# Kernel tuning notes

Hardware: AMD Instinct MI355X
Metric: run time of the kernel (lower is better)

Reference implementation:

```python
import jax, jax.numpy as jnp
import numpy as np

TAU = 2.0        # leak time constant
CLAMP = 1000.0   # state clamp in LeakyRNN.recurrence
EPS = 1e-4       # eps in PolicyRNN.evaluate

B, T, H, NI, NA = 64, 2048, 256, 4, 2


def setup_inputs() -> dict:
    key = jax.random.key(0)
    ks = jax.random.split(key, 10)
    state = jax.random.normal(ks[0], (B, T, NI), jnp.float32)
    last_action = jax.random.normal(ks[1], (B, T, NA), jnp.float32)
    reward = jax.random.randint(ks[2], (B, T, NA), 0, 2).astype(jnp.float32)
    hidden_in = jnp.zeros((B, H), jnp.float32)
    W1 = jax.random.normal(ks[3], (H, NI + 2 * NA), jnp.float32) * np.float32(np.sqrt(2.0 / (NI + 2 * NA)))
    b1 = jnp.zeros((H,), jnp.float32)
    Wih = jax.random.normal(ks[4], (H, H), jnp.float32) * np.float32(np.sqrt(2.0 / H))
    Whh_raw = jax.random.normal(ks[5], (H, H), jnp.float32) * np.float32(0.5 / np.sqrt(H))
    W2 = jax.random.normal(ks[6], (H, H), jnp.float32) * np.float32(np.sqrt(2.0 / H))
    b2 = jnp.zeros((H,), jnp.float32)
    W3 = jax.random.normal(ks[7], (NA, H), jnp.float32) * np.float32(np.sqrt(2.0 / H))
    b3 = jnp.zeros((NA,), jnp.float32)
    Qs = jax.random.normal(ks[8], (B, T, NA), jnp.float32)
    # MultLayerAdaptiveSimple with alphas=[1,0]: weight1=[1,0], weight2=[0,1]
    mix_w = jnp.array([[1.0, 0.0], [0.0, 1.0]], jnp.float32)
    return dict(state=state, last_action=last_action, reward=reward,
                hidden_in=hidden_in, W1=W1, b1=b1, Wih=Wih, Whh_raw=Whh_raw,
                W2=W2, b2=b2, W3=W3, b3=b3, Qs=Qs, mix_w=mix_w)


def reference(state, last_action, reward, hidden_in, W1, b1, Wih, Whh_raw,
              W2, b2, W3, b3, Qs, mix_w):
    # (B,T,.) -> (T,B,.) time-major, matching permute(1,0,2)
    x = jnp.concatenate([reward, state, last_action], -1).transpose(1, 0, 2)
    x = jax.nn.relu(x @ W1.T + b1)                     # linear1 + relu

    # IdentityDiagonal parametrization: zero diagonal, subtract I/tau
    Whh = Whh_raw - jnp.diag(jnp.diag(Whh_raw)) - jnp.eye(H, dtype=Whh_raw.dtype) / TAU
    u = x @ Wih.T                                      # precompute input drive (T,B,H)
    leak = 1.0 - 1.0 / TAU

    def step(h, ut):
        h_new = jnp.clip(leak * h + ut + jax.nn.relu(h) @ Whh.T, -CLAMP, CLAMP)
        return h_new, h_new

    hidden_out, ys = jax.lax.scan(step, hidden_in, u)  # ys: (T,B,H)

    y = jax.nn.relu(ys @ W2.T + b2) @ W3.T + b3        # linear2+relu, linear3
    probs = y.transpose(1, 0, 2)                       # (B,T,NA)

    # evaluate() deterministic path with reward-indexed adaptive mixing
    z = (probs == 0.0).astype(probs.dtype) * EPS
    logp = jnp.log(jax.nn.softmax(probs, -1) + z)
    logq = jnp.log(jax.nn.softmax(Qs, -1) + z)
    # SumOne parametrization (p=1) on each MultLayer 2-vector
    w = jnp.clip(mix_w, -1.0, 1.0)
    table = w / jnp.sum(jnp.abs(w), axis=1, keepdims=True)   # (2,2)
    sel = table[reward[:, :, 0].astype(jnp.int32)]           # (B,T,2)
    mixed = logp * sel[..., :1] + logq * sel[..., 1:2]
    return jnp.exp(mixed), hidden_out
```

## Files before the change

kernel.cpp:

```cpp
#include <hip/hip_runtime.h>
#include <hip/hip_bf16.h>
#include <math.h>

#define Bn 64
#define Tn 2048
#define Hn 256

constexpr float LEAK    = 0.5f;
constexpr float NEGDIAG = -0.5f;
constexpr float CLAMP_V = 1000.0f;
constexpr float EPS_V   = 1e-4f;

typedef __attribute__((ext_vector_type(8))) short  short8;
typedef __attribute__((ext_vector_type(4))) float  f32x4;
typedef __attribute__((ext_vector_type(2))) float  f32x2;

#define FAST_BARRIER() do {                                   \
    asm volatile("s_waitcnt lgkmcnt(0)" ::: "memory");        \
    __builtin_amdgcn_s_barrier();                             \
    asm volatile("" ::: "memory");                            \
  } while (0)

__device__ inline short bf16_rne(float x) {
  __hip_bfloat16 h = __float2bfloat16(x);
  return *reinterpret_cast<short*>(&h);
}
__device__ inline float bf16_to_f(short s) {
  union { unsigned u; float f; } c; c.u = ((unsigned)(unsigned short)s) << 16;
  return c.f;
}
__device__ inline unsigned pack2(short a, short b) {
  return (unsigned)(unsigned short)a | ((unsigned)(unsigned short)b << 16);
}
__device__ inline void pkfma(f32x2& a, f32x2 x, f32x2 y) {
  asm("v_pk_fma_f32 %0, %1, %2, %0" : "+v"(a) : "v"(x), "v"(y));
}
#define SWZ(x, imm) __int_as_float(__builtin_amdgcn_ds_swizzle(__float_as_int(x), (imm)))

#define SA 40

__global__ __launch_bounds__(512) void g_u(
    const float* __restrict__ reward, const float* __restrict__ state,
    const float* __restrict__ last_action, const float* __restrict__ W1,
    const float* __restrict__ b1, const float* __restrict__ Wih,
    float* __restrict__ u)
{
  __shared__ short Ah[128*SA], Al[128*SA], Bh[256*SA], Bl[256*SA];
  __shared__ __align__(16) float inp_s[128][8];
  __shared__ __align__(16) float w1_s[256][8];
  __shared__ float b1_s[256];
  const int tid = threadIdx.x;
  const int r0  = blockIdx.x * 128;

  for (int idx = tid; idx < 2048; idx += 512) ((float*)w1_s)[idx] = W1[idx];
  if (tid < 256) b1_s[tid] = b1[tid];
  for (int idx = tid; idx < 1024; idx += 512) {
    int rr = idx >> 3, i = idx & 7;
    int r = r0 + rr, b = r & 63, t = r >> 6;
    long base = (long)b * Tn + t;
    float v;
    if (i < 2)      v = reward[base * 2 + i];
    else if (i < 6) v = state[base * 4 + (i - 2)];
    else            v = last_action[base * 2 + (i - 6)];
    inp_s[rr][i] = v;
  }

  const int w    = tid >> 6, lane = tid & 63;
  const int wm   = w >> 2, wn = w & 3;
  const int fr   = lane & 15, fk = lane >> 4;
  f32x4 acc[4][4];
  #pragma unroll
  for (int a = 0; a < 4; ++a)
    #pragma unroll
    for (int c = 0; c < 4; ++c) acc[a][c] = (f32x4){0.f, 0.f, 0.f, 0.f};

  __syncthreads();

  for (int ks = 0; ks < 8; ++ks) {
    const int k0 = ks * 32;
    if (ks) __syncthreads();
    for (int p = tid; p < 2048; p += 512) {
      int rr = p >> 4, kp = (p & 15) * 2;
      int k = k0 + kp;
      float4 iv0 = *reinterpret_cast<const float4*>(&inp_s[rr][0]);
      float4 iv1 = *reinterpret_cast<const float4*>(&inp_s[rr][4]);
      float4 wa0 = *reinterpret_cast<const float4*>(&w1_s[k][0]);
      float4 wa1 = *reinterpret_cast<const float4*>(&w1_s[k][4]);
      float4 wb0 = *reinterpret_cast<const float4*>(&w1_s[k+1][0]);
      float4 wb1 = *reinterpret_cast<const float4*>(&w1_s[k+1][4]);
      float s0 = b1_s[k], s1 = b1_s[k+1];
      s0 = fmaf(iv0.x, wa0.x, s0); s0 = fmaf(iv0.y, wa0.y, s0);
      s0 = fmaf(iv0.z, wa0.z, s0); s0 = fmaf(iv0.w, wa0.w, s0);
      s0 = fmaf(iv1.x, wa1.x, s0); s0 = fmaf(iv1.y, wa1.y, s0);
      s0 = fmaf(iv1.z, wa1.z, s0); s0 = fmaf(iv1.w, wa1.w, s0);
      s1 = fmaf(iv0.x, wb0.x, s1); s1 = fmaf(iv0.y, wb0.y, s1);
      s1 = fmaf(iv0.z, wb0.z, s1); s1 = fmaf(iv0.w, wb0.w, s1);
      s1 = fmaf(iv1.x, wb1.x, s1); s1 = fmaf(iv1.y, wb1.y, s1);
      s1 = fmaf(iv1.z, wb1.z, s1); s1 = fmaf(iv1.w, wb1.w, s1);
      float v0 = fmaxf(s0, 0.f), v1 = fmaxf(s1, 0.f);
      short h0 = bf16_rne(v0), h1 = bf16_rne(v1);
      short l0 = bf16_rne(v0 - bf16_to_f(h0)), l1 = bf16_rne(v1 - bf16_to_f(h1));
      int off = rr * SA + kp;
      *reinterpret_cast<unsigned*>(&Ah[off]) = pack2(h0, h1);
      *reinterpret_cast<unsigned*>(&Al[off]) = pack2(l0, l1);
    }
    for (int c = tid; c < 2048; c += 512) {
      int n = c >> 3, kc = (c & 7) * 4;
      float4 f = *reinterpret_cast<const float4*>(&Wih[n * 256 + k0 + kc]);
      short h0 = bf16_rne(f.x), h1 = bf16_rne(f.y), h2 = bf16_rne(f.z), h3 = bf16_rne(f.w);
      short l0 = bf16_rne(f.x - bf16_to_f(h0)), l1 = bf16_rne(f.y - bf16_to_f(h1));
      short l2 = bf16_rne(f.z - bf16_to_f(h2)), l3 = bf16_rne(f.w - bf16_to_f(h3));
      int off = n * SA + kc;
      *reinterpret_cast<uint2*>(&Bh[off]) = make_uint2(pack2(h0, h1), pack2(h2, h3));
      *reinterpret_cast<uint2*>(&Bl[off]) = make_uint2(pack2(l0, l1), pack2(l2, l3));
    }
    __syncthreads();
    short8 bhf[4], blf[4];
    #pragma unroll
    for (int nf = 0; nf < 4; ++nf) {
      const int brow = wn * 64 + nf * 16 + fr;
      bhf[nf] = *reinterpret_cast<const short8*>(&Bh[brow * SA + fk * 8]);
      blf[nf] = *reinterpret_cast<const short8*>(&Bl[brow * SA + fk * 8]);
    }
    #pragma unroll
    for (int mf = 0; mf < 4; ++mf) {
      const int arow = wm * 64 + mf * 16 + fr;
      short8 ah = *reinterpret_cast<const short8*>(&Ah[arow * SA + fk * 8]);
      short8 al = *reinterpret_cast<const short8*>(&Al[arow * SA + fk * 8]);
      #pragma unroll
      for (int nf = 0; nf < 4; ++nf) {
        acc[mf][nf] = __builtin_amdgcn_mfma_f32_16x16x32_bf16(ah, bhf[nf], acc[mf][nf], 0, 0, 0);
        acc[mf][nf] = __builtin_amdgcn_mfma_f32_16x16x32_bf16(ah, blf[nf], acc[mf][nf], 0, 0, 0);
        acc[mf][nf] = __builtin_amdgcn_mfma_f32_16x16x32_bf16(al, bhf[nf], acc[mf][nf], 0, 0, 0);
      }
    }
  }
  #pragma unroll
  for (int mf = 0; mf < 4; ++mf) {
    const int rbase = r0 + wm * 64 + mf * 16 + (lane >> 4) * 4;
    #pragma unroll
    for (int nf = 0; nf < 4; ++nf) {
      const int n = wn * 64 + nf * 16 + fr;
      #pragma unroll
      for (int j = 0; j < 4; ++j)
        u[(long)(rbase + j) * Hn + n] = acc[mf][nf][j];
    }
  }
}

__global__ __launch_bounds__(1024, 4) void k_scan(
    const float* __restrict__ Whh_raw, const float* __restrict__ hidden_in,
    float* __restrict__ ubuf, float* __restrict__ out)
{
  __shared__ __align__(16) float rh[2][256];
  const int tid = threadIdx.x;
  const int w = tid >> 6;
  const int l = tid & 63;
  const int g = l & 15;
  const int o = l >> 4;
  const int b = blockIdx.x;
  const int kbase = g << 4;

  f32x2 w2[4][8];
  #pragma unroll
  for (int m = 0; m < 4; ++m) {
    const int j = (w << 4) + (o << 2) + m;
    #pragma unroll
    for (int i = 0; i < 8; ++i) {
      const int k = kbase + i * 2;
      float a = Whh_raw[j * 256 + k];
      float c = Whh_raw[j * 256 + k + 1];
      if (k == j)     a = NEGDIAG;
      if (k + 1 == j) c = NEGDIAG;
      w2[m][i] = (f32x2){a, c};
    }
  }

  const int b0 = g & 1, b1 = (g >> 1) & 1;
  const bool owner = (g < 4);
  const int m_own = (b0 << 1) | b1;
  const int j_own = (w << 4) + (o << 2) + m_own;

  const int wr_off = (j_own & ~15) | ((((j_own >> 2) + (j_own >> 5)) & 3) << 2)
                   | (j_own & 3);
  int a_q[4];
  #pragma unroll
  for (int q = 0; q < 4; ++q) a_q[q] = kbase + (((((g >> 1) + q) & 3)) << 2);

  float h = 0.f, u_c = 0.f, u_n = 0.f;
  if (owner) {
    h   = hidden_in[b * Hn + j_own];
    u_c = ubuf[b * Hn + j_own];
    u_n = ubuf[((long)Bn + b) * Hn + j_own];
  }
  const float* u_ptr  = ubuf + ((long)2 * Bn + b) * Hn + j_own;
  float*       ys_ptr = ubuf + (long)b * Hn + j_own;

#define SCAN_STEP(P)                                                         \
  {                                                                          \
    if (owner) rh[P][wr_off] = fmaxf(h, 0.f);                                \
    FAST_BARRIER();                                                          \
    float u_pf = 0.f;                                                        \
    if (owner && t + 2 < Tn) u_pf = *u_ptr;                                  \
    float4 r[4];                                                             \
    r[0] = *reinterpret_cast<const float4*>(&rh[P][a_q[0]]);                 \
    r[1] = *reinterpret_cast<const float4*>(&rh[P][a_q[1]]);                 \
    r[2] = *reinterpret_cast<const float4*>(&rh[P][a_q[2]]);                 \
    r[3] = *reinterpret_cast<const float4*>(&rh[P][a_q[3]]);                 \
    f32x2 c0 = {0.f, 0.f}, c1 = {0.f, 0.f}, c2 = {0.f, 0.f}, c3 = {0.f, 0.f};\
    _Pragma("unroll")                                                        \
    for (int q = 0; q < 4; ++q) {                                            \
      const f32x2 rlo = {r[q].x, r[q].y};                                    \
      const f32x2 rhi = {r[q].z, r[q].w};                                    \
      pkfma(c0, rlo, w2[0][2*q]); pkfma(c0, rhi, w2[0][2*q+1]);              \
      pkfma(c1, rlo, w2[1][2*q]); pkfma(c1, rhi, w2[1][2*q+1]);              \
      pkfma(c2, rlo, w2[2][2*q]); pkfma(c2, rhi, w2[2][2*q+1]);              \
      pkfma(c3, rlo, w2[3][2*q]); pkfma(c3, rhi, w2[3][2*q+1]);              \
    }                                                                        \
    const float v0 = c0.x + c0.y, v1 = c1.x + c1.y;                          \
    const float v2 = c2.x + c2.y, v3 = c3.x + c3.y;                          \
    const float s00 = b0 ? v0 : v2;                                          \
    const float k00 = b0 ? v2 : v0;                                          \
    const float s01 = b0 ? v1 : v3;                                          \
    const float k01 = b0 ? v3 : v1;                                          \
    const float t00 = k00 + SWZ(s00, 0x041F);                                \
    const float t01 = k01 + SWZ(s01, 0x041F);                                \
    const float s1 = b1 ? t00 : t01;                                         \
    const float k1 = b1 ? t01 : t00;                                         \
    float s = k1 + SWZ(s1, 0x081F);                                          \
    s += SWZ(s, 0x101F);                                                     \
    s += SWZ(s, 0x201F);                                                     \
    if (owner) {                                                             \
      float hn = fmaf(LEAK, h, u_c) + s;                                     \
      hn = fminf(fmaxf(hn, -CLAMP_V), CLAMP_V);                              \
      *ys_ptr = hn;                                                          \
      h = hn; u_c = u_n; u_n = u_pf;                                         \
    }                                                                        \
    ys_ptr += Bn * Hn;                                                       \
    u_ptr  += Bn * Hn;                                                       \
  }

  for (int tt = 0; tt < Tn; tt += 2) {
    { const int t = tt;     SCAN_STEP(0) }
    { const int t = tt + 1; SCAN_STEP(1) }
  }
#undef SCAN_STEP

  if (owner) out[(long)Bn * Tn * 2 + b * Hn + j_own] = h;
}

__global__ __launch_bounds__(512) void g_out(
    const float* __restrict__ ys, const float* __restrict__ W2,
    const float* __restrict__ b2, const float* __restrict__ W3,
    float* __restrict__ yout)
{
  __shared__ short Ah[128*SA], Al[128*SA], Bh[256*SA], Bl[256*SA];
  __shared__ float b2_s[256];
  __shared__ float w3_s[512];
  const int tid = threadIdx.x;
  const int r0  = blockIdx.x * 128;

  if (tid < 256) b2_s[tid] = b2[tid];
  if (tid < 512) w3_s[tid] = W3[tid];

  const int w    = tid >> 6, lane = tid & 63;
  const int wm   = w >> 2, wn = w & 3;
  const int fr   = lane & 15, fk = lane >> 4;
  f32x4 acc[4][4];
  #pragma unroll
  for (int a = 0; a < 4; ++a)
    #pragma unroll
    for (int c = 0; c < 4; ++c) acc[a][c] = (f32x4){0.f, 0.f, 0.f, 0.f};

  __syncthreads();

  for (int ks = 0; ks < 8; ++ks) {
    const int k0 = ks * 32;
    if (ks) __syncthreads();
    for (int c = tid; c < 1024; c += 512) {
      int rr = c >> 3, kc = (c & 7) * 4;
      float4 f = *reinterpret_cast<const float4*>(&ys[(long)(r0 + rr) * Hn + k0 + kc]);
      short h0 = bf16_rne(f.x), h1 = bf16_rne(f.y), h2 = bf16_rne(f.z), h3 = bf16_rne(f.w);
      short l0 = bf16_rne(f.x - bf16_to_f(h0)), l1 = bf16_rne(f.y - bf16_to_f(h1));
      short l2 = bf16_rne(f.z - bf16_to_f(h2)), l3 = bf16_rne(f.w - bf16_to_f(h3));
      int off = rr * SA + kc;
      *reinterpret_cast<uint2*>(&Ah[off]) = make_uint2(pack2(h0, h1), pack2(h2, h3));
      *reinterpret_cast<uint2*>(&Al[off]) = make_uint2(pack2(l0, l1), pack2(l2, l3));
    }
    for (int c = tid; c < 2048; c += 512) {
      int n = c >> 3, kc = (c & 7) * 4;
      float4 f = *reinterpret_cast<const float4*>(&W2[n * 256 + k0 + kc]);
      short h0 = bf16_rne(f.x), h1 = bf16_rne(f.y), h2 = bf16_rne(f.z), h3 = bf16_rne(f.w);
      short l0 = bf16_rne(f.x - bf16_to_f(h0)), l1 = bf16_rne(f.y - bf16_to_f(h1));
      short l2 = bf16_rne(f.z - bf16_to_f(h2)), l3 = bf16_rne(f.w - bf16_to_f(h3));
      int off = n * SA + kc;
      *reinterpret_cast<uint2*>(&Bh[off]) = make_uint2(pack2(h0, h1), pack2(h2, h3));
      *reinterpret_cast<uint2*>(&Bl[off]) = make_uint2(pack2(l0, l1), pack2(l2, l3));
    }
    __syncthreads();
    short8 bhf[4], blf[4];
    #pragma unroll
    for (int nf = 0; nf < 4; ++nf) {
      const int brow = wn * 64 + nf * 16 + fr;
      bhf[nf] = *reinterpret_cast<const short8*>(&Bh[brow * SA + fk * 8]);
      blf[nf] = *reinterpret_cast<const short8*>(&Bl[brow * SA + fk * 8]);
    }
    #pragma unroll
    for (int mf = 0; mf < 4; ++mf) {
      const int arow = wm * 64 + mf * 16 + fr;
      short8 ah = *reinterpret_cast<const short8*>(&Ah[arow * SA + fk * 8]);
      short8 al = *reinterpret_cast<const short8*>(&Al[arow * SA + fk * 8]);
      #pragma unroll
      for (int nf = 0; nf < 4; ++nf) {
        acc[mf][nf] = __builtin_amdgcn_mfma_f32_16x16x32_bf16(ah, bhf[nf], acc[mf][nf], 0, 0, 0);
        acc[mf][nf] = __builtin_amdgcn_mfma_f32_16x16x32_bf16(ah, blf[nf], acc[mf][nf], 0, 0, 0);
        acc[mf][nf] = __builtin_amdgcn_mfma_f32_16x16x32_bf16(al, bhf[nf], acc[mf][nf], 0, 0, 0);
      }
    }
  }

  float yp[4][4][2];
  #pragma unroll
  for (int mf = 0; mf < 4; ++mf)
    #pragma unroll
    for (int j = 0; j < 4; ++j) { yp[mf][j][0] = 0.f; yp[mf][j][1] = 0.f; }

  #pragma unroll
  for (int mf = 0; mf < 4; ++mf)
    #pragma unroll
    for (int nf = 0; nf < 4; ++nf) {
      const int n = wn * 64 + nf * 16 + fr;
      const float b2v = b2_s[n];
      const float w30 = w3_s[n], w31 = w3_s[256 + n];
      #pragma unroll
      for (int j = 0; j < 4; ++j) {
        float v = fmaxf(acc[mf][nf][j] + b2v, 0.f);
        yp[mf][j][0] = fmaf(v, w30, yp[mf][j][0]);
        yp[mf][j][1] = fmaf(v, w31, yp[mf][j][1]);
      }
    }
  #pragma unroll
  for (int off = 1; off < 16; off <<= 1) {
    #pragma unroll
    for (int mf = 0; mf < 4; ++mf)
      #pragma unroll
      for (int j = 0; j < 4; ++j) {
        yp[mf][j][0] += __shfl_xor(yp[mf][j][0], off);
        yp[mf][j][1] += __shfl_xor(yp[mf][j][1], off);
      }
  }

  __syncthreads();
  float* yred = reinterpret_cast<float*>(Ah);
  if (fr == 0) {
    #pragma unroll
    for (int mf = 0; mf < 4; ++mf)
      #pragma unroll
      for (int j = 0; j < 4; ++j) {
        int rl = wm * 64 + mf * 16 + (lane >> 4) * 4 + j;
        yred[(rl * 2 + 0) * 4 + wn] = yp[mf][j][0];
        yred[(rl * 2 + 1) * 4 + wn] = yp[mf][j][1];
      }
  }
  __syncthreads();
  if (tid < 256) {
    int rl = tid >> 1, a = tid & 1;
    const float* yr = &yred[(rl * 2 + a) * 4];
    float y = (yr[0] + yr[1]) + (yr[2] + yr[3]);
    int r = r0 + rl, b = r & 63, t = r >> 6;
    yout[((long)b * Tn + t) * 2 + a] = y;
  }
}

__global__ __launch_bounds__(256) void k_head(
    float* __restrict__ out, const float* __restrict__ Qs,
    const float* __restrict__ reward, const float* __restrict__ mix_w,
    const float* __restrict__ b3)
{
  const int idx = blockIdx.x * 256 + threadIdx.x;
  if (idx >= Bn * Tn) return;
  const long base = (long)idx * 2;
  float y0 = out[base]     + b3[0];
  float y1 = out[base + 1] + b3[1];
  float z0 = (y0 == 0.f) ? EPS_V : 0.f;
  float z1 = (y1 == 0.f) ? EPS_V : 0.f;

  float m  = fmaxf(y0, y1);
  float e0 = expf(y0 - m), e1 = expf(y1 - m), es = e0 + e1;
  float sp0 = e0 / es, sp1 = e1 / es;

  float q0 = Qs[base], q1 = Qs[base + 1];
  float mq = fmaxf(q0, q1);
  float f0 = expf(q0 - mq), f1 = expf(q1 - mq), fs = f0 + f1;
  float sq0 = f0 / fs, sq1 = f1 / fs;

  int ri = (int)reward[base];
  float m0 = fminf(fmaxf(mix_w[ri * 2 + 0], -1.f), 1.f);
  float m1 = fminf(fmaxf(mix_w[ri * 2 + 1], -1.f), 1.f);
  float den = fabsf(m0) + fabsf(m1);
  float s0 = m0 / den, s1 = m1 / den;

  out[base]     = expf(s0 * logf(sp0 + z0) + s1 * logf(sq0 + z0));
  out[base + 1] = expf(s0 * logf(sp1 + z1) + s1 * logf(sq1 + z1));
}

extern "C" void kernel_launch(void* const* d_in, const int* in_sizes, int n_in,
                              void* d_out, int out_size, void* d_ws, size_t ws_size,
                              hipStream_t stream)
{
  const float* state       = (const float*)d_in[0];
  const float* last_action = (const float*)d_in[1];
  const float* reward      = (const float*)d_in[2];
  const float* hidden_in   = (const float*)d_in[3];
  const float* W1          = (const float*)d_in[4];
  const float* b1          = (const float*)d_in[5];
  const float* Wih         = (const float*)d_in[6];
  const float* Whh_raw     = (const float*)d_in[7];
  const float* W2          = (const float*)d_in[8];
  const float* b2          = (const float*)d_in[9];
  const float* W3          = (const float*)d_in[10];
  const float* b3          = (const float*)d_in[11];
  const float* Qs          = (const float*)d_in[12];
  const float* mix_w       = (const float*)d_in[13];
  float* out = (float*)d_out;
  float* u   = (float*)d_ws;

  const int nrows = Tn * Bn;
  g_u   <<<nrows / 128, 512, 0, stream>>>(reward, state, last_action, W1, b1, Wih, u);
  k_scan<<<Bn,          1024, 0, stream>>>(Whh_raw, hidden_in, u, out);
  g_out <<<nrows / 128, 512, 0, stream>>>(u, W2, b2, W3, out);
  k_head<<<nrows / 256, 256, 0, stream>>>(out, Qs, reward, mix_w, b3);
}
```

Baseline: 1.638 ms.

## Halve scan block to 512 threads with 16 outputs per lane and DPP reduction

The recurrent scan kernel now runs 8 waves of 64 lanes per batch element instead of 16 waves. Each lane holds 16 output rows by 8 columns of Whh in registers instead of 4 by 16. The cross-lane reduction becomes a transpose-style butterfly using DPP row moves, one swizzle and a permlane32 swap, so each step needs fewer barrier participants and fewer LDS swizzles. The trade-off is higher register pressure per lane, with 128 weight floats held in registers, and a more intricate LDS read and write layout.

```diff
diff --git a/kernel.cpp b/kernel.cpp
--- a/kernel.cpp
+++ b/kernel.cpp
@@ -36,6 +36,12 @@
   asm("v_pk_fma_f32 %0, %1, %2, %0" : "+v"(a) : "v"(x), "v"(y));
 }
 #define SWZ(x, imm) __int_as_float(__builtin_amdgcn_ds_swizzle(__float_as_int(x), (imm)))
+
+template <int CTRL>
+__device__ __forceinline__ float dpp_recv(float x) {
+  return __int_as_float(
+      __builtin_amdgcn_update_dpp(0, __float_as_int(x), CTRL, 0xF, 0xF, true));
+}
 
 #define SA 40
 
@@ -148,7 +154,7 @@
   }
 }
 
-__global__ __launch_bounds__(1024, 4) void k_scan(
+__global__ __launch_bounds__(512, 2) void k_scan(
     const float* __restrict__ Whh_raw, const float* __restrict__ hidden_in,
     float* __restrict__ ubuf, float* __restrict__ out)
 {
@@ -156,41 +162,40 @@
   const int tid = threadIdx.x;
   const int w = tid >> 6;
   const int l = tid & 63;
-  const int g = l & 15;
-  const int o = l >> 4;
+  const int g = (l & 3) | ((l >> 1) & 0x1C);
+  const int o = (l >> 2) & 1;
   const int b = blockIdx.x;
-  const int kbase = g << 4;
-
-  f32x2 w2[4][8];
-  #pragma unroll
-  for (int m = 0; m < 4; ++m) {
-    const int j = (w << 4) + (o << 2) + m;
-    #pragma unroll
-    for (int i = 0; i < 8; ++i) {
-      const int k = kbase + i * 2;
+  const int key = ((g & 1) << 3) | ((g & 2) << 1) | ((g & 4) >> 1) | ((g & 8) >> 3);
+
+  f32x2 w2[16][4];
+  #pragma unroll
+  for (int s = 0; s < 16; ++s) {
+    const int j = (w << 5) + (o << 4) + (s ^ key);
+    #pragma unroll
+    for (int i = 0; i < 4; ++i) {
+      const int k = (g << 3) + 2 * i;
       float a = Whh_raw[j * 256 + k];
       float c = Whh_raw[j * 256 + k + 1];
       if (k == j)     a = NEGDIAG;
       if (k + 1 == j) c = NEGDIAG;
-      w2[m][i] = (f32x2){a, c};
-    }
-  }
-
-  const int b0 = g & 1, b1 = (g >> 1) & 1;
-  const bool owner = (g < 4);
-  const int m_own = (b0 << 1) | b1;
-  const int j_own = (w << 4) + (o << 2) + m_own;
-
-  const int wr_off = (j_own & ~15) | ((((j_own >> 2) + (j_own >> 5)) & 3) << 2)
-                   | (j_own & 3);
-  int a_q[4];
-  #pragma unroll
-  for (int q = 0; q < 4; ++q) a_q[q] = kbase + (((((g >> 1) + q) & 3)) << 2);
+      w2[s][i] = (f32x2){a, c};
+    }
+  }
+
+  const bool owner = (l < 32);
+  const int j_own = (w << 5) + (o << 4) + key;
+
+  const int row  = g >> 2;
+  const int srot = (((g & 3) << 3) + (row << 2)) & 31;
+  const int rd1  = row * 32 + srot;
+  const int rd2  = row * 32 + ((srot + 4) & 31);
+  const int wrow = j_own >> 5;
+  const int wr   = wrow * 32 + (((j_own & 31) + (wrow << 2)) & 31);
 
   float h = 0.f, u_c = 0.f, u_n = 0.f;
   if (owner) {
     h   = hidden_in[b * Hn + j_own];
-    u_c = ubuf[b * Hn + j_own];
+    u_c = ubuf[(long)b * Hn + j_own];
     u_n = ubuf[((long)Bn + b) * Hn + j_own];
   }
   const float* u_ptr  = ubuf + ((long)2 * Bn + b) * Hn + j_own;
@@ -198,40 +203,36 @@
 
 #define SCAN_STEP(P)                                                         \
   {                                                                          \
-    if (owner) rh[P][wr_off] = fmaxf(h, 0.f);                                \
+    if (owner) rh[P][wr] = fmaxf(h, 0.f);                                    \
     FAST_BARRIER();                                                          \
     float u_pf = 0.f;                                                        \
     if (owner && t + 2 < Tn) u_pf = *u_ptr;                                  \
-    float4 r[4];                                                             \
-    r[0] = *reinterpret_cast<const float4*>(&rh[P][a_q[0]]);                 \
-    r[1] = *reinterpret_cast<const float4*>(&rh[P][a_q[1]]);                 \
-    r[2] = *reinterpret_cast<const float4*>(&rh[P][a_q[2]]);                 \
-    r[3] = *reinterpret_cast<const float4*>(&rh[P][a_q[3]]);                 \
-    f32x2 c0 = {0.f, 0.f}, c1 = {0.f, 0.f}, c2 = {0.f, 0.f}, c3 = {0.f, 0.f};\
+    const float4 ra = *reinterpret_cast<const float4*>(&rh[P][rd1]);         \
+    const float4 rb = *reinterpret_cast<const float4*>(&rh[P][rd2]);         \
+    const f32x2 rp0 = {ra.x, ra.y}, rp1 = {ra.z, ra.w};                      \
+    const f32x2 rp2 = {rb.x, rb.y}, rp3 = {rb.z, rb.w};                      \
+    float v[16];                                                             \
     _Pragma("unroll")                                                        \
-    for (int q = 0; q < 4; ++q) {                                            \
-      const f32x2 rlo = {r[q].x, r[q].y};                                    \
-      const f32x2 rhi = {r[q].z, r[q].w};                                    \
-      pkfma(c0, rlo, w2[0][2*q]); pkfma(c0, rhi, w2[0][2*q+1]);              \
-      pkfma(c1, rlo, w2[1][2*q]); pkfma(c1, rhi, w2[1][2*q+1]);              \
-      pkfma(c2, rlo, w2[2][2*q]); pkfma(c2, rhi, w2[2][2*q+1]);              \
-      pkfma(c3, rlo, w2[3][2*q]); pkfma(c3, rhi, w2[3][2*q+1]);              \
+    for (int s = 0; s < 16; ++s) {                                           \
+      f32x2 c = {0.f, 0.f};                                                  \
+      pkfma(c, rp0, w2[s][0]); pkfma(c, rp1, w2[s][1]);                      \
+      pkfma(c, rp2, w2[s][2]); pkfma(c, rp3, w2[s][3]);                      \
+      v[s] = c.x + c.y;                                                      \
     }                                                                        \
-    const float v0 = c0.x + c0.y, v1 = c1.x + c1.y;                          \
-    const float v2 = c2.x + c2.y, v3 = c3.x + c3.y;                          \
-    const float s00 = b0 ? v0 : v2;                                          \
-    const float k00 = b0 ? v2 : v0;                                          \
-    const float s01 = b0 ? v1 : v3;                                          \
-    const float k01 = b0 ? v3 : v1;                                          \
-    const float t00 = k00 + SWZ(s00, 0x041F);                                \
-    const float t01 = k01 + SWZ(s01, 0x041F);                                \
-    const float s1 = b1 ? t00 : t01;                                         \
-    const float k1 = b1 ? t01 : t00;                                         \
-    float s = k1 + SWZ(s1, 0x081F);                                          \
-    s += SWZ(s, 0x101F);                                                     \
-    s += SWZ(s, 0x201F);                                                     \
+    _Pragma("unroll")                                                        \
+    for (int s = 0; s < 8; ++s) v[s] += dpp_recv<0xB1>(v[s + 8]);            \
+    _Pragma("unroll")                                                        \
+    for (int s = 0; s < 4; ++s) v[s] += dpp_recv<0x4E>(v[s + 4]);            \
+    _Pragma("unroll")                                                        \
+    for (int s = 0; s < 2; ++s) v[s] += dpp_recv<0x128>(v[s + 2]);           \
+    v[0] += SWZ(v[1], 0x401F);                                               \
+    {                                                                        \
+      float pa = v[0], pb = v[0];                                            \
+      asm("v_permlane32_swap_b32 %0, %1" : "+v"(pa), "+v"(pb));              \
+      v[0] = pa + pb;                                                        \
+    }                                                                        \
     if (owner) {                                                             \
-      float hn = fmaf(LEAK, h, u_c) + s;                                     \
+      float hn = fmaf(LEAK, h, u_c) + v[0];                                  \
       hn = fminf(fmaxf(hn, -CLAMP_V), CLAMP_V);                              \
       *ys_ptr = hn;                                                          \
       h = hn; u_c = u_n; u_n = u_pf;                                         \
@@ -427,7 +428,7 @@
 
   const int nrows = Tn * Bn;
   g_u   <<<nrows / 128, 512, 0, stream>>>(reward, state, last_action, W1, b1, Wih, u);
-  k_scan<<<Bn,          1024, 0, stream>>>(Whh_raw, hidden_in, u, out);
+  k_scan<<<Bn,           512, 0, stream>>>(Whh_raw, hidden_in, u, out);
   g_out <<<nrows / 128, 512, 0, stream>>>(u, W2, b2, W3, out);
   k_head<<<nrows / 256, 256, 0, stream>>>(out, Qs, reward, mix_w, b3);
 }
```

After: 1.462 ms. 10.8% less time.
